# Optimization experiments

Hardware: AMD Instinct MI355X
Metric: run time of the kernel (lower is better)

Reference implementation:

```python
import jax, jax.numpy as jnp
import numpy as np

B, R, C1, C2, C3, K, NC = 512, 200, 32, 32, 512, 8, 2
RATIO = 0.5
K1 = int(np.ceil(RATIO * R))    # 100 nodes kept after pool1
K2 = int(np.ceil(RATIO * K1))   # 50 nodes kept after pool2
EDGE_P = 0.1
NEG = -1e9
BN_EPS = 1e-5
LEAK = 0.01


def setup_inputs() -> dict:
    key = jax.random.key(0)
    ks = jax.random.split(key, 12)

    def lin_w(k, o, i):
        return (jax.random.normal(k, (o, i)) / np.sqrt(i)).astype(jnp.float32)

    return {
        "x": jax.random.normal(ks[0], (B, R, R), dtype=jnp.float32),
        "adj": jax.random.uniform(ks[1], (B, R, R), dtype=jnp.float32),
        "roi": jnp.arange(R, dtype=jnp.int32),
        # conv1 ROI-conditioned weight net: Linear(R->K) -> ReLU -> Linear(K->R*C1)
        "W1a": lin_w(ks[2], K, R), "b1a": jnp.zeros((K,), jnp.float32),
        "W2a": lin_w(ks[3], R * C1, K), "b2a": jnp.zeros((R * C1,), jnp.float32),
        "bias1": jnp.zeros((C1,), jnp.float32),
        # conv2 ROI-conditioned weight net: Linear(R->K) -> ReLU -> Linear(K->C1*C2)
        "W1b": lin_w(ks[4], K, R), "b1b": jnp.zeros((K,), jnp.float32),
        "W2b": lin_w(ks[5], C1 * C2, K), "b2b": jnp.zeros((C1 * C2,), jnp.float32),
        "bias2": jnp.zeros((C2,), jnp.float32),
        # TopK pooling projection vectors
        "wp1": jax.random.normal(ks[6], (C1,), dtype=jnp.float32),
        "wp2": jax.random.normal(ks[7], (C2,), dtype=jnp.float32),
        # MLP head
        "Wm1": lin_w(ks[8], C2, (C1 + C2) * 2), "bm1": jnp.zeros((C2,), jnp.float32),
        "g1": jnp.ones((C2,), jnp.float32), "be1": jnp.zeros((C2,), jnp.float32),
        "Wm2": lin_w(ks[9], C3, C2), "bm2": jnp.zeros((C3,), jnp.float32),
        "g2": jnp.ones((C3,), jnp.float32), "be2": jnp.zeros((C3,), jnp.float32),
        "Ws": lin_w(ks[10], NC, C3), "bs": jnp.zeros((NC,), jnp.float32),
    }


def _nn_table(W1, b1, W2, b2, cin, cout):
    # nn applied to one-hot ROI vectors == table lookup; build the full [R, cin, cout] table once.
    t = jax.nn.relu(W1.T + b1) @ W2.T + b2  # [R, cin*cout]
    return t.reshape(R, cin, cout)


def _gconv(x, w_adj, mask, w_node, bias):
    # per-node ROI-conditioned transform, then edge-softmax weighted aggregation
    if w_node.ndim == 3:   # shared table indexed by arange -> [R,cin,cout]
        xt = jnp.einsum('bni,nio->bno', x, w_node)
    else:                   # gathered per graph -> [B,n,cin,cout]
        xt = jnp.einsum('bni,bnio->bno', x, w_node)
    n = x.shape[1]
    eye = jnp.eye(n, dtype=bool)
    # remove self loops, add self loop with weight 1, softmax over incoming edges
    logits = jnp.where(mask & ~eye, w_adj, NEG)
    logits = jnp.where(eye, 1.0, logits)
    att = jax.nn.softmax(logits, axis=-1)  # row i = incoming edges of node i
    return jnp.einsum('bij,bjo->bio', att, xt) + bias


def _topk_pool(h, w_adj, mask, roi, w, k):
    s = jax.nn.sigmoid(h @ w / jnp.linalg.norm(w))  # [B, n]
    vals, perm = jax.lax.top_k(s, k)
    xs = jnp.take_along_axis(h, perm[:, :, None], axis=1) * vals[:, :, None]
    b = jnp.arange(h.shape[0])[:, None, None]
    w_sub = w_adj[b, perm[:, :, None], perm[:, None, :]]
    m_sub = mask[b, perm[:, :, None], perm[:, None, :]]
    roi_sub = roi[perm] if roi.ndim == 1 else jnp.take_along_axis(roi, perm, axis=1)
    return xs, w_sub, m_sub, roi_sub, vals


def _augment(w_adj, mask):
    # add_self_loops(fill=1) -> spspmm(A, A) -> remove_self_loops, in dense-batched form
    n = w_adj.shape[1]
    eye = jnp.eye(n, dtype=bool)
    wd = jnp.where(mask & ~eye, w_adj, 0.0)
    wd = jnp.where(eye, 1.0, wd)
    a2 = jnp.einsum('bij,bjk->bik', wd, wd)
    m2 = (a2 != 0.0) & ~eye
    a2 = jnp.where(eye, 0.0, a2)
    return a2, m2


def _mlp_block(y, Wl, bl, g, be):
    y = y @ Wl.T + bl
    y = jnp.where(y > 0, y, LEAK * y)          # LeakyReLU(0.01)
    mu = jnp.mean(y, axis=0)
    var = jnp.var(y, axis=0)                    # training-mode BatchNorm1d
    return g * (y - mu) * jax.lax.rsqrt(var + BN_EPS) + be


def _forward(x, adj, roi, W1a, b1a, W2a, b2a, bias1, W1b, b1b, W2b, b2b, bias2,
             wp1, wp2, Wm1, bm1, g1, be1, Wm2, bm2, g2, be2, Ws, bs):
    mask0 = adj < EDGE_P
    wtab1 = _nn_table(W1a, b1a, W2a, b2a, R, C1)   # [R, R, C1]
    h1 = _gconv(x, adj, mask0, wtab1[roi], bias1)  # [B, R, C1]
    x1, w1, m1, roi1, vals1 = _topk_pool(h1, adj, mask0, roi, wp1, K1)
    a_aug, m_aug = _augment(w1, m1)                 # 2-hop augmented adjacency
    wtab2 = _nn_table(W1b, b1b, W2b, b2b, C1, C2)  # [R, C1, C2]
    h2 = _gconv(x1, a_aug, m_aug, wtab2[roi1], bias2)  # [B, K1, C2]
    x2, _, _, _, vals2 = _topk_pool(h2, a_aug, m_aug, roi1, wp2, K2)
    # readout: [gmp, gap] per level, concatenated -> (C1+C2)*2 = 128
    feat = jnp.concatenate([x1.max(1), x1.mean(1), x2.max(1), x2.mean(1)], axis=-1)
    y = _mlp_block(feat, Wm1, bm1, g1, be1)
    y = _mlp_block(y, Wm2, bm2, g2, be2)
    logp = jax.nn.log_softmax(y @ Ws.T + bs, axis=-1)
    return logp, jax.nn.sigmoid(vals1), jax.nn.sigmoid(vals2)


def reference(x, adj, roi, W1a, b1a, W2a, b2a, bias1, W1b, b1b, W2b, b2b, bias2,
              wp1, wp2, Wm1, bm1, g1, be1, Wm2, bm2, g2, be2, Ws, bs):
    logp, s1, s2 = _forward(x, adj, roi, W1a, b1a, W2a, b2a, bias1,
                            W1b, b1b, W2b, b2b, bias2, wp1, wp2,
                            Wm1, bm1, g1, be1, Wm2, bm2, g2, be2, Ws, bs)
    return (logp, wp1, wp2, s1, s2)
```

## Files before the change

### kernel.cpp

```cpp
#include <hip/hip_runtime.h>
#include <math.h>

#define NB 512
#define RR 200
#define KK1 100
#define KK2 50

__device__ __forceinline__ float sigm(float v) { return 1.0f / (1.0f + expf(-v)); }

__global__ void k_tab(const float* __restrict__ W1, const float* __restrict__ b1,
                      const float* __restrict__ W2, const float* __restrict__ b2,
                      float* __restrict__ tab, int OUT) {
  int n = blockIdx.x;
  __shared__ float h[8];
  if (threadIdx.x < 8) {
    float v = W1[threadIdx.x * RR + n] + b1[threadIdx.x];
    h[threadIdx.x] = v > 0.f ? v : 0.f;
  }
  __syncthreads();
  for (int j = threadIdx.x; j < OUT; j += 256) {
    float acc = b2[j];
#pragma unroll
    for (int k = 0; k < 8; k++) acc += h[k] * W2[j * 8 + k];
    tab[(size_t)n * OUT + j] = acc;
  }
}

__global__ void k_norm(const float* __restrict__ wp1, const float* __restrict__ wp2,
                       float* __restrict__ norms) {
  int t = threadIdx.x;
  float a = (t < 32) ? wp1[t] * wp1[t] : 0.f;
  float b = (t < 32) ? wp2[t] * wp2[t] : 0.f;
  for (int s = 32; s; s >>= 1) { a += __shfl_xor(a, s); b += __shfl_xor(b, s); }
  if (t == 0) { norms[0] = sqrtf(a); norms[1] = sqrtf(b); }
}

__global__ __launch_bounds__(1024) void k_xt1(const float* __restrict__ x,
                                              const float* __restrict__ wtab1,
                                              float* __restrict__ xt1) {
  int n = blockIdx.x, t = threadIdx.x;
  __shared__ float wsm[6400];
  for (int idx = t; idx < 1600; idx += 1024)
    *(float4*)&wsm[idx * 4] = *(const float4*)(wtab1 + (size_t)n * 6400 + idx * 4);
  __syncthreads();
  int bg = t >> 3, og = t & 7;
  int b0 = bg * 4;
  const float* xp = x + (size_t)b0 * 40000 + (size_t)n * 200;
  float acc[4][4] = {};
  float4 A[4], Bf[4], N0[4] = {}, N1[4] = {};
#pragma unroll
  for (int r = 0; r < 4; r++) A[r] = *(const float4*)(xp + (size_t)r * 40000);
#pragma unroll
  for (int r = 0; r < 4; r++) Bf[r] = *(const float4*)(xp + (size_t)r * 40000 + 4);
  for (int g = 0; g < 50; g += 2) {
    int i = g * 4;
    if (g + 2 < 50) {
#pragma unroll
      for (int r = 0; r < 4; r++) N0[r] = *(const float4*)(xp + (size_t)r * 40000 + i + 8);
#pragma unroll
      for (int r = 0; r < 4; r++) N1[r] = *(const float4*)(xp + (size_t)r * 40000 + i + 12);
    }
#pragma unroll
    for (int k = 0; k < 4; k++) {
      float4 w4 = *(const float4*)&wsm[(i + k) * 32 + og * 4];
#pragma unroll
      for (int r = 0; r < 4; r++) {
        float xs = (&A[r].x)[k];
        acc[r][0] += xs * w4.x; acc[r][1] += xs * w4.y;
        acc[r][2] += xs * w4.z; acc[r][3] += xs * w4.w;
      }
    }
#pragma unroll
    for (int k = 0; k < 4; k++) {
      float4 w4 = *(const float4*)&wsm[(i + 4 + k) * 32 + og * 4];
#pragma unroll
      for (int r = 0; r < 4; r++) {
        float xs = (&Bf[r].x)[k];
        acc[r][0] += xs * w4.x; acc[r][1] += xs * w4.y;
        acc[r][2] += xs * w4.z; acc[r][3] += xs * w4.w;
      }
    }
#pragma unroll
    for (int r = 0; r < 4; r++) { A[r] = N0[r]; Bf[r] = N1[r]; }
  }
#pragma unroll
  for (int r = 0; r < 4; r++)
    *(float4*)(xt1 + (size_t)(b0 + r) * 6400 + (size_t)n * 32 + og * 4) =
        make_float4(acc[r][0], acc[r][1], acc[r][2], acc[r][3]);
}

__global__ __launch_bounds__(1024) void k_att1(const float* __restrict__ adj,
                                               const float* __restrict__ xt1,
                                               const float* __restrict__ bias1,
                                               const float* __restrict__ wp1,
                                               const float* __restrict__ norms,
                                               float* __restrict__ h1, float* __restrict__ sc1,
                                               int* __restrict__ perm1,
                                               float* __restrict__ vals1,
                                               float* __restrict__ out_s1) {
  int t = threadIdx.x;
  __shared__ float2 pvj[16][8][49];
  __shared__ int cntS[16][8];
  int w = t >> 6, lane = t & 63;
  int rq = lane >> 3, og = lane & 7;
  float4 bias4 = *(const float4*)(bias1 + og * 4);
  float4 wp4 = *(const float4*)(wp1 + og * 4);
  float nrm = norms[0];
  unsigned long long ltmask = (1ull << lane) - 1ull;
  int npass = (w < 9) ? 2 : 1;
  int total = 2 * npass;
  float av[8][4];
  {
    const float* abase = adj + (size_t)(blockIdx.x * 2) * 40000 + (size_t)(w * 8) * 200;
#pragma unroll
    for (int r = 0; r < 8; r++)
#pragma unroll
      for (int s2 = 0; s2 < 4; s2++) {
        int j = lane + 64 * s2;
        av[r][s2] = (j < RR) ? __builtin_nontemporal_load(abase + r * 200 + j) : 1.0f;
      }
  }
  for (int idx = 0; idx < total; idx++) {
    int second = (idx >= npass) ? 1 : 0;
    int b = blockIdx.x * 2 + second;
    int pass = idx - second * npass;
    int r0 = pass * 128 + w * 8;
#pragma unroll
    for (int r = 0; r < 8; r++) {
      int i = r0 + r;
      float e[4];
      bool nz[4];
#pragma unroll
      for (int s2 = 0; s2 < 4; s2++) {
        int j = lane + 64 * s2;
        float a = av[r][s2];
        bool keep = (j < RR) && ((j == i) || (a < 0.1f));
        float lg = (j == i) ? 1.0f : a;
        e[s2] = keep ? __expf(lg - 1.0f) : 0.f;
        nz[s2] = keep;
      }
      int base = 0;
#pragma unroll
      for (int s2 = 0; s2 < 4; s2++) {
        unsigned long long m = __ballot(nz[s2]);
        if (nz[s2]) pvj[w][r][base + __popcll(m & ltmask)] = make_float2(e[s2], (float)(lane + 64 * s2));
        base += __popcll(m);
      }
      if (lane == 0) cntS[w][r] = base;
    }
    if (idx + 1 < total) {
      int idx2 = idx + 1;
      int sec2 = (idx2 >= npass) ? 1 : 0;
      int b2 = blockIdx.x * 2 + sec2;
      int r02 = (idx2 - sec2 * npass) * 128 + w * 8;
      const float* abase = adj + (size_t)b2 * 40000 + (size_t)r02 * 200;
#pragma unroll
      for (int r = 0; r < 8; r++)
#pragma unroll
        for (int s2 = 0; s2 < 4; s2++) {
          int j = lane + 64 * s2;
          if (j < RR) av[r][s2] = __builtin_nontemporal_load(abase + r * 200 + j);
        }
    }
    int cnt = cntS[w][rq];
    const float* xtb = xt1 + (size_t)b * 6400 + og * 4;
    float a0 = 0.f, a1 = 0.f, a2 = 0.f, a3 = 0.f, lsum = 0.f;
    for (int q = 0; q < cnt; q++) {
      float2 pe = pvj[w][rq][q];
      int jj = (int)pe.y;
      float4 xv = *(const float4*)(xtb + jj * 32);
      lsum += pe.x;
      a0 += pe.x * xv.x; a1 += pe.x * xv.y; a2 += pe.x * xv.z; a3 += pe.x * xv.w;
    }
    float inv = 1.0f / lsum;
    int i = r0 + rq;
    float4 h4 = make_float4(a0 * inv + bias4.x, a1 * inv + bias4.y,
                            a2 * inv + bias4.z, a3 * inv + bias4.w);
    *(float4*)(h1 + ((size_t)b * RR + i) * 32 + og * 4) = h4;
    float tt = h4.x * wp4.x + h4.y * wp4.y + h4.z * wp4.z + h4.w * wp4.w;
    tt += __shfl_xor(tt, 1); tt += __shfl_xor(tt, 2); tt += __shfl_xor(tt, 4);
    if (og == 0) sc1[b * RR + i] = sigm(tt / nrm);
  }
  float* sc = (float*)&pvj[0][0][0];
  for (int bb = 0; bb < 2; bb++) {
    int b = blockIdx.x * 2 + bb;
    __syncthreads();
    if (t < RR) sc[t] = sc1[b * RR + t];
    __syncthreads();
    if (t < RR) {
      float si = sc[t];
      int rank = 0;
      for (int j = 0; j < RR; j++) {
        float sj = sc[j];
        rank += (sj > si) || (sj == si && j < t);
      }
      if (rank < KK1) {
        perm1[b * KK1 + rank] = t;
        vals1[b * KK1 + rank] = si;
        out_s1[b * KK1 + rank] = sigm(si);
      }
    }
  }
}

__global__ __launch_bounds__(256) void k_stage2a(const float* __restrict__ h1,
                                                 const float* __restrict__ wtab2,
                                                 const int* __restrict__ perm1,
                                                 const float* __restrict__ vals1,
                                                 float* __restrict__ xt2,
                                                 float* __restrict__ feat) {
  int b = blockIdx.x, t = threadIdx.x;
  int kbase = blockIdx.y * 50;
  __shared__ float x1s[KK1 * 33];
  __shared__ int pk[KK1];
  __shared__ float vk[KK1];
  if (t < KK1) { pk[t] = perm1[b * KK1 + t]; vk[t] = vals1[b * KK1 + t]; }
  __syncthreads();
  for (int i = t; i < KK1 * 32; i += 256) {
    int k = i >> 5, o = i & 31;
    x1s[k * 33 + o] = h1[((size_t)b * RR + pk[k]) * 32 + o] * vk[k];
  }
  __syncthreads();
  if (blockIdx.y == 0 && t < 32) {
    float mx = -3e38f, sm = 0.f;
    for (int k = 0; k < KK1; k++) { float v = x1s[k * 33 + t]; mx = fmaxf(mx, v); sm += v; }
    feat[b * 128 + t] = mx;
    feat[b * 128 + 32 + t] = sm / 100.0f;
  }
  int w = t >> 6, lane = t & 63;
  int og = lane & 7, kq = lane >> 3;
#pragma unroll
  for (int pass = 0; pass < 2; pass++) {
    int kl = pass * 32 + w * 8 + kq;
    if (kl < 50) {
      int kg = kbase + kl;
      const float* W = wtab2 + (size_t)pk[kg] * 1024 + og * 4;
      float4 a4 = make_float4(0.f, 0.f, 0.f, 0.f);
#pragma unroll 8
      for (int ii = 0; ii < 32; ii++) {
        float4 w4 = *(const float4*)(W + ii * 32);
        float xs = x1s[kg * 33 + ii];
        a4.x += xs * w4.x; a4.y += xs * w4.y; a4.z += xs * w4.z; a4.w += xs * w4.w;
      }
      *(float4*)(xt2 + (size_t)b * 3200 + kg * 32 + og * 4) = a4;
    }
  }
}

__global__ __launch_bounds__(256) void k_wd(const float* __restrict__ adj,
                                            const int* __restrict__ perm1,
                                            float* __restrict__ wd) {
  int b = blockIdx.x, t = threadIdx.x;
  int g0 = blockIdx.y * 20;
  __shared__ float rowbuf[20][200];
  __shared__ int pk[KK1];
  if (t < KK1) pk[t] = perm1[b * KK1 + t];
  __syncthreads();
  for (int idx = t; idx < 4000; idx += 256) {
    int r = idx / 200, j = idx - r * 200;
    rowbuf[r][j] = adj[(size_t)b * 40000 + (size_t)pk[g0 + r] * 200 + j];
  }
  __syncthreads();
  for (int idx = t; idx < 2000; idx += 256) {
    int r = idx / 100, k2 = idx - r * 100;
    int k1 = g0 + r;
    float v;
    if (k1 == k2) v = 1.0f;
    else {
      float av = rowbuf[r][pk[k2]];
      v = (av < 0.1f) ? av : 0.0f;
    }
    wd[(size_t)b * (KK1 * KK1) + k1 * KK1 + k2] = v;
  }
}

__global__ __launch_bounds__(512) void k_stage2b(const float* __restrict__ wd,
                                                 const float* __restrict__ xt2,
                                                 const float* __restrict__ bias2,
                                                 const float* __restrict__ wp2,
                                                 const float* __restrict__ norms,
                                                 float* __restrict__ h2, float* __restrict__ sc2,
                                                 float* __restrict__ out_s2,
                                                 float* __restrict__ feat) {
  int b = blockIdx.x, t = threadIdx.x;
  __shared__ float wds[KK1][100];
  __shared__ float xts[KK1 * 32];
  __shared__ float pT[8][KK1][4];
  __shared__ int   nzidx[KK1][36];
  int w = t >> 6, lane = t & 63;
  unsigned long long ltmask = (1ull << lane) - 1ull;
  float bias_o = bias2[lane & 31];
  float wp_o = wp2[lane & 31];
  float nrm = norms[1];
  int k2a = lane;
  int k2b = lane + 64;
  bool vb = k2b < KK1;
  for (int i = t; i < KK1 * KK1; i += 512) ((float*)wds)[i] = wd[(size_t)b * (KK1 * KK1) + i];
  for (int idx = t; idx < 800; idx += 512)
    *(float4*)&xts[idx * 4] = *(const float4*)(xt2 + (size_t)b * 3200 + idx * 4);
  __syncthreads();
  for (int r = w; r < KK1; r += 8) {
    bool nz0 = (wds[r][lane] != 0.f);
    bool nz1 = (lane < KK1 - 64) && (wds[r][64 + lane] != 0.f);
    unsigned long long m0 = __ballot(nz0);
    unsigned long long m1 = __ballot(nz1);
    int c0 = __popcll(m0);
    int cnt = c0 + __popcll(m1);
    if (nz0) nzidx[r][__popcll(m0 & ltmask)] = lane;
    if (nz1) nzidx[r][c0 + __popcll(m1 & ltmask)] = 64 + lane;
    int pad = (4 - (cnt & 3)) & 3;
    if (lane < pad) nzidx[r][cnt + lane] = 0;
    if (lane == 0) nzidx[r][35] = cnt;
  }
  __syncthreads();
  for (int g = w; g < 25; g += 8) {
    int r0 = g * 4;
    float acc[4][2];
#pragma unroll
    for (int r = 0; r < 4; r++) {
      int k1 = r0 + r;
      int cnt = nzidx[k1][35];
      float s0 = 0.f, s1 = 0.f;
      for (int it = 0; it < cnt; it += 4) {
        int4 m4 = *(const int4*)&nzidx[k1][it];
        float a0 = wds[k1][m4.x];
        float a1 = (it + 1 < cnt) ? wds[k1][m4.y] : 0.f;
        float a2v = (it + 2 < cnt) ? wds[k1][m4.z] : 0.f;
        float a3 = (it + 3 < cnt) ? wds[k1][m4.w] : 0.f;
        s0 += a0 * wds[m4.x][k2a]; s1 += a0 * wds[m4.x][k2b];
        s0 += a1 * wds[m4.y][k2a]; s1 += a1 * wds[m4.y][k2b];
        s0 += a2v * wds[m4.z][k2a]; s1 += a2v * wds[m4.z][k2b];
        s0 += a3 * wds[m4.w][k2a]; s1 += a3 * wds[m4.w][k2b];
      }
      acc[r][0] = s0; acc[r][1] = s1;
    }
    float p0[4], p1[4], rs[4];
#pragma unroll
    for (int r = 0; r < 4; r++) {
      int k1 = r0 + r;
      float lv0 = (k1 == k2a) ? 1.0f : ((acc[r][0] != 0.0f) ? acc[r][0] : -1e9f);
      float lv1 = (k1 == k2b) ? 1.0f : ((acc[r][1] != 0.0f) ? acc[r][1] : -1e9f);
      float mx = vb ? fmaxf(lv0, lv1) : lv0;
      for (int s = 32; s; s >>= 1) mx = fmaxf(mx, __shfl_xor(mx, s));
      float e0 = expf(lv0 - mx);
      float e1 = vb ? expf(lv1 - mx) : 0.f;
      float ls = e0 + e1;
      for (int s = 32; s; s >>= 1) ls += __shfl_xor(ls, s);
      p0[r] = e0; p1[r] = e1; rs[r] = 1.0f / ls;
    }
    *(float4*)&pT[w][k2a][0] = make_float4(p0[0] * rs[0], p0[1] * rs[1], p0[2] * rs[2], p0[3] * rs[3]);
    if (vb) *(float4*)&pT[w][k2b][0] = make_float4(p1[0] * rs[0], p1[1] * rs[1], p1[2] * rs[2], p1[3] * rs[3]);
    int half = lane >> 5, o = lane & 31;
    float hv[4] = {0.f, 0.f, 0.f, 0.f};
    for (int jj = 0; jj < 50; jj++) {
      int j = half * 50 + jj;
      float4 pv = *(const float4*)&pT[w][j][0];
      float xv = xts[j * 32 + o];
      hv[0] += pv.x * xv; hv[1] += pv.y * xv; hv[2] += pv.z * xv; hv[3] += pv.w * xv;
    }
#pragma unroll
    for (int r = 0; r < 4; r++) hv[r] += __shfl_down(hv[r], 32);
    if (lane < 32) {
#pragma unroll
      for (int r = 0; r < 4; r++) {
        float h = hv[r] + bias_o;
        h2[((size_t)b * KK1 + (r0 + r)) * 32 + o] = h;
        float tt = h * wp_o;
        for (int s = 16; s; s >>= 1) tt += __shfl_xor(tt, s);
        if (lane == 0) sc2[b * KK1 + (r0 + r)] = sigm(tt / nrm);
      }
    }
  }
  __syncthreads();
  float* s = (float*)&pT[0][0][0];
  int* p2 = (int*)(s + 128);
  float* v2 = (float*)(p2 + 64);
  if (t < KK1) s[t] = sc2[b * KK1 + t];
  __syncthreads();
  if (t < KK1) {
    float si = s[t];
    int rank = 0;
    for (int j = 0; j < KK1; j++) {
      float sj = s[j];
      rank += (sj > si) || (sj == si && j < t);
    }
    if (rank < KK2) {
      p2[rank] = t;
      v2[rank] = si;
      out_s2[b * KK2 + rank] = sigm(si);
    }
  }
  __syncthreads();
  if (t < 32) {
    float mx = -3e38f, sm = 0.f;
    for (int k = 0; k < KK2; k++) {
      float v = h2[((size_t)b * KK1 + p2[k]) * 32 + t] * v2[k];
      mx = fmaxf(mx, v);
      sm += v;
    }
    feat[b * 128 + 64 + t] = mx;
    feat[b * 128 + 96 + t] = sm / 50.0f;
  }
}

__global__ void k_mlp1(const float* __restrict__ feat, const float* __restrict__ Wm1,
                       const float* __restrict__ bm1, float* __restrict__ y1) {
  __shared__ float Wt[128 * 32];
  __shared__ float f[8][128];
  int t = threadIdx.x;
  for (int i = t; i < 4096; i += 256) { int c = i >> 7, d = i & 127; Wt[d * 32 + c] = Wm1[i]; }
  int b0 = blockIdx.x * 8;
  for (int i = t; i < 1024; i += 256) f[i >> 7][i & 127] = feat[b0 * 128 + i];
  __syncthreads();
  int bl = t >> 5, c = t & 31;
  float acc = bm1[c];
#pragma unroll 4
  for (int d = 0; d < 128; d++) acc += f[bl][d] * Wt[d * 32 + c];
  y1[(b0 + bl) * 32 + c] = acc > 0.f ? acc : 0.01f * acc;
}

__global__ void k_bn(const float* __restrict__ y, int C, float* __restrict__ stats) {
  int c = blockIdx.x, t = threadIdx.x;
  __shared__ float ys[512];
  __shared__ float red[8];
  ys[t] = y[(size_t)t * C + c];
  ys[t + 256] = y[(size_t)(t + 256) * C + c];
  __syncthreads();
  float s = ys[t] + ys[t + 256];
  for (int d = 32; d; d >>= 1) s += __shfl_xor(s, d);
  if ((t & 63) == 0) red[t >> 6] = s;
  __syncthreads();
  float mu = (red[0] + red[1] + red[2] + red[3]) * (1.0f / 512.0f);
  float d0 = ys[t] - mu, d1 = ys[t + 256] - mu;
  float v = d0 * d0 + d1 * d1;
  for (int d = 32; d; d >>= 1) v += __shfl_xor(v, d);
  if ((t & 63) == 0) red[4 + (t >> 6)] = v;
  __syncthreads();
  if (t == 0) {
    float var = (red[4] + red[5] + red[6] + red[7]) * (1.0f / 512.0f);
    stats[c] = mu;
    stats[C + c] = rsqrtf(var + 1e-5f);
  }
}

__global__ void k_mlp2(const float* __restrict__ y1, const float* __restrict__ st1,
                       const float* __restrict__ g1, const float* __restrict__ be1,
                       const float* __restrict__ Wm2, const float* __restrict__ bm2,
                       float* __restrict__ y2) {
  __shared__ float yn[32];
  int b = blockIdx.x, t = threadIdx.x;
  if (t < 32) {
    float v = y1[b * 32 + t];
    yn[t] = g1[t] * (v - st1[t]) * st1[32 + t] + be1[t];
  }
  __syncthreads();
  for (int c = t; c < 512; c += 256) {
    float acc = bm2[c];
#pragma unroll
    for (int k = 0; k < 32; k++) acc += yn[k] * Wm2[c * 32 + k];
    y2[(size_t)b * 512 + c] = acc > 0.f ? acc : 0.01f * acc;
  }
}

__global__ void k_final(const float* __restrict__ y2, const float* __restrict__ st2,
                        const float* __restrict__ g2, const float* __restrict__ be2,
                        const float* __restrict__ Ws, const float* __restrict__ bs,
                        float* __restrict__ out) {
  int w = threadIdx.x >> 6, lane = threadIdx.x & 63;
  int b = blockIdx.x * 4 + w;
  float z0 = 0.f, z1 = 0.f;
  for (int c = lane; c < 512; c += 64) {
    float v = g2[c] * (y2[(size_t)b * 512 + c] - st2[c]) * st2[512 + c] + be2[c];
    z0 += v * Ws[c];
    z1 += v * Ws[512 + c];
  }
  for (int s = 32; s; s >>= 1) { z0 += __shfl_xor(z0, s); z1 += __shfl_xor(z1, s); }
  if (lane == 0) {
    z0 += bs[0];
    z1 += bs[1];
    float m = fmaxf(z0, z1);
    float lse = m + logf(expf(z0 - m) + expf(z1 - m));
    out[b * 2] = z0 - lse;
    out[b * 2 + 1] = z1 - lse;
  }
}

__global__ void k_copy(const float* __restrict__ wp1, const float* __restrict__ wp2,
                       float* __restrict__ out) {
  int t = threadIdx.x;
  if (t < 32) out[1024 + t] = wp1[t];
  else if (t < 64) out[1056 + (t - 32)] = wp2[t - 32];
}

extern "C" void kernel_launch(void* const* d_in, const int* in_sizes, int n_in,
                              void* d_out, int out_size, void* d_ws, size_t ws_size,
                              hipStream_t stream) {
  const float* x    = (const float*)d_in[0];
  const float* adj  = (const float*)d_in[1];
  const float* W1a  = (const float*)d_in[3];
  const float* b1a  = (const float*)d_in[4];
  const float* W2a  = (const float*)d_in[5];
  const float* b2a  = (const float*)d_in[6];
  const float* bias1= (const float*)d_in[7];
  const float* W1b  = (const float*)d_in[8];
  const float* b1b  = (const float*)d_in[9];
  const float* W2b  = (const float*)d_in[10];
  const float* b2b  = (const float*)d_in[11];
  const float* bias2= (const float*)d_in[12];
  const float* wp1  = (const float*)d_in[13];
  const float* wp2  = (const float*)d_in[14];
  const float* Wm1  = (const float*)d_in[15];
  const float* bm1  = (const float*)d_in[16];
  const float* g1   = (const float*)d_in[17];
  const float* be1  = (const float*)d_in[18];
  const float* Wm2  = (const float*)d_in[19];
  const float* bm2  = (const float*)d_in[20];
  const float* g2   = (const float*)d_in[21];
  const float* be2  = (const float*)d_in[22];
  const float* Ws   = (const float*)d_in[23];
  const float* bs   = (const float*)d_in[24];
  float* out = (float*)d_out;

  float* ws = (float*)d_ws;
  float* WTAB1 = ws;
  float* WTAB2 = WTAB1 + 1280000;
  float* NORMS = WTAB2 + 204800;
  float* XT1   = NORMS + 16;
  float* H1    = XT1 + 3276800;
  float* SC1   = H1 + 3276800;
  float* VALS1 = SC1 + 102400;
  int*   PERM1 = (int*)(VALS1 + 51200);
  float* XT2   = (float*)(PERM1 + 51200);
  float* WD    = XT2 + 1638400;
  float* H2    = WD + 5120000;
  float* SC2   = H2 + 1638400;
  float* FEAT  = SC2 + 51200;
  float* Y1    = FEAT + 65536;
  float* ST1   = Y1 + 16384;
  float* Y2    = ST1 + 64;
  float* ST2   = Y2 + 262144;

  k_tab<<<200, 256, 0, stream>>>(W1a, b1a, W2a, b2a, WTAB1, 6400);
  k_tab<<<200, 256, 0, stream>>>(W1b, b1b, W2b, b2b, WTAB2, 1024);
  k_norm<<<1, 64, 0, stream>>>(wp1, wp2, NORMS);
  k_xt1<<<200, 1024, 0, stream>>>(x, WTAB1, XT1);
  k_att1<<<256, 1024, 0, stream>>>(adj, XT1, bias1, wp1, NORMS, H1, SC1,
                                   PERM1, VALS1, out + 1088);
  k_stage2a<<<dim3(512, 2), 256, 0, stream>>>(H1, WTAB2, PERM1, VALS1, XT2, FEAT);
  k_wd<<<dim3(512, 5), 256, 0, stream>>>(adj, PERM1, WD);
  k_stage2b<<<512, 512, 0, stream>>>(WD, XT2, bias2, wp2, NORMS, H2, SC2,
                                     out + 52288, FEAT);
  k_mlp1<<<64, 256, 0, stream>>>(FEAT, Wm1, bm1, Y1);
  k_bn<<<32, 256, 0, stream>>>(Y1, 32, ST1);
  k_mlp2<<<512, 256, 0, stream>>>(Y1, ST1, g1, be1, Wm2, bm2, Y2);
  k_bn<<<512, 256, 0, stream>>>(Y2, 512, ST2);
  k_final<<<128, 256, 0, stream>>>(Y2, ST2, g2, be2, Ws, bs, out);
  k_copy<<<1, 64, 0, stream>>>(wp1, wp2, out);
}
```

Measured before the change: 205.8 us.

## Split att1 into one-graph-per-block attention and separate top-k kernel

```diff
diff --git a/kernel.cpp b/kernel.cpp
--- a/kernel.cpp
+++ b/kernel.cpp
@@ -94,40 +94,32 @@
                                                const float* __restrict__ bias1,
                                                const float* __restrict__ wp1,
                                                const float* __restrict__ norms,
-                                               float* __restrict__ h1, float* __restrict__ sc1,
-                                               int* __restrict__ perm1,
-                                               float* __restrict__ vals1,
-                                               float* __restrict__ out_s1) {
+                                               float* __restrict__ h1, float* __restrict__ sc1) {
   int t = threadIdx.x;
-  __shared__ float2 pvj[16][8][49];
-  __shared__ int cntS[16][8];
+  __shared__ float2 pvj[16][4][49];
+  __shared__ int cntS[16][4];
   int w = t >> 6, lane = t & 63;
-  int rq = lane >> 3, og = lane & 7;
-  float4 bias4 = *(const float4*)(bias1 + og * 4);
-  float4 wp4 = *(const float4*)(wp1 + og * 4);
+  int rq = lane >> 4, cg = lane & 15;
+  float2 biasv = *(const float2*)(bias1 + cg * 2);
+  float2 wpv = *(const float2*)(wp1 + cg * 2);
   float nrm = norms[0];
   unsigned long long ltmask = (1ull << lane) - 1ull;
-  int npass = (w < 9) ? 2 : 1;
-  int total = 2 * npass;
-  float av[8][4];
+  int b = blockIdx.x;
+  float av[4][4];
   {
-    const float* abase = adj + (size_t)(blockIdx.x * 2) * 40000 + (size_t)(w * 8) * 200;
-#pragma unroll
-    for (int r = 0; r < 8; r++)
+    const float* abase = adj + (size_t)b * 40000 + (size_t)(w * 4) * 200;
+#pragma unroll
+    for (int r = 0; r < 4; r++)
 #pragma unroll
       for (int s2 = 0; s2 < 4; s2++) {
         int j = lane + 64 * s2;
         av[r][s2] = (j < RR) ? __builtin_nontemporal_load(abase + r * 200 + j) : 1.0f;
       }
   }
-  for (int idx = 0; idx < total; idx++) {
-    int second = (idx >= npass) ? 1 : 0;
-    int b = blockIdx.x * 2 + second;
-    int pass = idx - second * npass;
-    int r0 = pass * 128 + w * 8;
-#pragma unroll
-    for (int r = 0; r < 8; r++) {
-      int i = r0 + r;
+  for (int rg = w; rg < 50; rg += 16) {
+#pragma unroll
+    for (int r = 0; r < 4; r++) {
+      int i = rg * 4 + r;
       float e[4];
       bool nz[4];
 #pragma unroll
@@ -148,14 +140,11 @@
       }
       if (lane == 0) cntS[w][r] = base;
     }
-    if (idx + 1 < total) {
-      int idx2 = idx + 1;
-      int sec2 = (idx2 >= npass) ? 1 : 0;
-      int b2 = blockIdx.x * 2 + sec2;
-      int r02 = (idx2 - sec2 * npass) * 128 + w * 8;
-      const float* abase = adj + (size_t)b2 * 40000 + (size_t)r02 * 200;
-#pragma unroll
-      for (int r = 0; r < 8; r++)
+    int rg2 = rg + 16;
+    if (rg2 < 50) {
+      const float* abase = adj + (size_t)b * 40000 + (size_t)(rg2 * 4) * 200;
+#pragma unroll
+      for (int r = 0; r < 4; r++)
 #pragma unroll
         for (int s2 = 0; s2 < 4; s2++) {
           int j = lane + 64 * s2;
@@ -163,42 +152,44 @@
         }
     }
     int cnt = cntS[w][rq];
-    const float* xtb = xt1 + (size_t)b * 6400 + og * 4;
-    float a0 = 0.f, a1 = 0.f, a2 = 0.f, a3 = 0.f, lsum = 0.f;
+    const float* xtb = xt1 + (size_t)b * 6400 + cg * 2;
+    float ax = 0.f, ay = 0.f, lsum = 0.f;
     for (int q = 0; q < cnt; q++) {
       float2 pe = pvj[w][rq][q];
       int jj = (int)pe.y;
-      float4 xv = *(const float4*)(xtb + jj * 32);
+      float2 xv = *(const float2*)(xtb + jj * 32);
       lsum += pe.x;
-      a0 += pe.x * xv.x; a1 += pe.x * xv.y; a2 += pe.x * xv.z; a3 += pe.x * xv.w;
+      ax += pe.x * xv.x;
+      ay += pe.x * xv.y;
     }
     float inv = 1.0f / lsum;
-    int i = r0 + rq;
-    float4 h4 = make_float4(a0 * inv + bias4.x, a1 * inv + bias4.y,
-                            a2 * inv + bias4.z, a3 * inv + bias4.w);
-    *(float4*)(h1 + ((size_t)b * RR + i) * 32 + og * 4) = h4;
-    float tt = h4.x * wp4.x + h4.y * wp4.y + h4.z * wp4.z + h4.w * wp4.w;
-    tt += __shfl_xor(tt, 1); tt += __shfl_xor(tt, 2); tt += __shfl_xor(tt, 4);
-    if (og == 0) sc1[b * RR + i] = sigm(tt / nrm);
-  }
-  float* sc = (float*)&pvj[0][0][0];
-  for (int bb = 0; bb < 2; bb++) {
-    int b = blockIdx.x * 2 + bb;
-    __syncthreads();
-    if (t < RR) sc[t] = sc1[b * RR + t];
-    __syncthreads();
-    if (t < RR) {
-      float si = sc[t];
-      int rank = 0;
-      for (int j = 0; j < RR; j++) {
-        float sj = sc[j];
-        rank += (sj > si) || (sj == si && j < t);
-      }
-      if (rank < KK1) {
-        perm1[b * KK1 + rank] = t;
-        vals1[b * KK1 + rank] = si;
-        out_s1[b * KK1 + rank] = sigm(si);
-      }
+    int i = rg * 4 + rq;
+    float2 hv = make_float2(ax * inv + biasv.x, ay * inv + biasv.y);
+    *(float2*)(h1 + ((size_t)b * RR + i) * 32 + cg * 2) = hv;
+    float tt = hv.x * wpv.x + hv.y * wpv.y;
+    tt += __shfl_xor(tt, 1); tt += __shfl_xor(tt, 2);
+    tt += __shfl_xor(tt, 4); tt += __shfl_xor(tt, 8);
+    if (cg == 0) sc1[b * RR + i] = sigm(tt / nrm);
+  }
+}
+
+__global__ void k_top1(const float* __restrict__ sc1, int* __restrict__ perm1,
+                       float* __restrict__ vals1, float* __restrict__ out_s1) {
+  int b = blockIdx.x, t = threadIdx.x;
+  __shared__ float s[RR];
+  for (int i = t; i < RR; i += 256) s[i] = sc1[b * RR + i];
+  __syncthreads();
+  for (int i = t; i < RR; i += 256) {
+    float si = s[i];
+    int rank = 0;
+    for (int j = 0; j < RR; j++) {
+      float sj = s[j];
+      rank += (sj > si) || (sj == si && j < i);
+    }
+    if (rank < KK1) {
+      perm1[b * KK1 + rank] = i;
+      vals1[b * KK1 + rank] = si;
+      out_s1[b * KK1 + rank] = sigm(si);
     }
   }
 }
@@ -544,8 +535,8 @@
   k_tab<<<200, 256, 0, stream>>>(W1b, b1b, W2b, b2b, WTAB2, 1024);
   k_norm<<<1, 64, 0, stream>>>(wp1, wp2, NORMS);
   k_xt1<<<200, 1024, 0, stream>>>(x, WTAB1, XT1);
-  k_att1<<<256, 1024, 0, stream>>>(adj, XT1, bias1, wp1, NORMS, H1, SC1,
-                                   PERM1, VALS1, out + 1088);
+  k_att1<<<512, 1024, 0, stream>>>(adj, XT1, bias1, wp1, NORMS, H1, SC1);
+  k_top1<<<512, 256, 0, stream>>>(SC1, PERM1, VALS1, out + 1088);
   k_stage2a<<<dim3(512, 2), 256, 0, stream>>>(H1, WTAB2, PERM1, VALS1, XT2, FEAT);
   k_wd<<<dim3(512, 5), 256, 0, stream>>>(adj, PERM1, WD);
   k_stage2b<<<512, 512, 0, stream>>>(WD, XT2, bias2, wp2, NORMS, H2, SC2,
```

Measured after the change: 202.4 us, median of 2. No clear change (-1.7%).
